# Performance work log

Measured on AMD Instinct MI355X. Metric: run time of the kernel, lower is better.

## Reference

```python
import jax, jax.numpy as jnp
import numpy as np

H = 8  # number of heads


def setup_inputs() -> dict:
    key0 = jax.random.key(0)
    ks = jax.random.split(key0, 10)
    B, Lq, Lk = 2, 256, 512
    q_model = k_model = v_model = d_model = 512
    d_k = d_model // H
    s = 0.02
    return {
        "query": jax.random.normal(ks[0], (B, Lq, q_model), jnp.float32),
        "key": jax.random.normal(ks[1], (B, Lk, k_model), jnp.float32),
        "value": jax.random.normal(ks[2], (B, Lk, v_model), jnp.float32),
        "mask": jax.random.randint(ks[3], (B, Lk), 0, 2, jnp.int32),
        # weights stored as (in, out) so projection is x @ W
        "Wq": jax.random.normal(ks[4], (q_model, d_model), jnp.float32) * s,
        "Wk": jax.random.normal(ks[5], (k_model, d_model), jnp.float32) * s,
        "Wv": jax.random.normal(ks[6], (v_model, d_model), jnp.float32) * s,
        "Wo": jax.random.normal(ks[7], (d_model, d_model), jnp.float32) * s,
        "wa": jax.random.normal(ks[8], (d_k,), jnp.float32) * s,
    }


def reference(query, key, value, mask, Wq, Wk, Wv, Wo, wa):
    B, Lq, _ = query.shape
    Lk = key.shape[1]
    d_model = Wq.shape[1]
    d_k = d_model // H

    def split_heads(x, W, L):
        return (x @ W).reshape(B, L, H, d_k).transpose(0, 2, 1, 3)  # (B,H,L,dk)

    q = split_heads(query, Wq, Lq)
    k = split_heads(key, Wk, Lk)
    v = split_heads(value, Wv, Lk)

    # additive (Bahdanau) scores: tanh(q_i + k_j) . wa  -> (B,H,Lq,Lk)
    feats = jnp.tanh(q[:, :, :, None, :] + k[:, :, None, :, :])
    scores = jnp.einsum("bhqkd,d->bhqk", feats, wa)

    scores = jnp.where(mask[:, None, None, :] == 0, jnp.float32(-1e9), scores)
    weights = jax.nn.softmax(scores, axis=-1)

    x = jnp.einsum("bhqk,bhkd->bhqd", weights, v)
    x = x.transpose(0, 2, 1, 3).reshape(B, Lq, H * d_k)
    return x @ Wo
```

## Files before the change

kernel.cpp:

```cpp
#include <hip/hip_runtime.h>

#define NB 2
#define LQ 256
#define LK 512
#define DM 512
#define NH 8
#define ROWS 4
#define C2F 2.885390081777927f
#define L2E 1.4426950408889634f

typedef __attribute__((ext_vector_type(8))) short short8;
typedef __attribute__((ext_vector_type(4))) float f32x4;

__device__ __forceinline__ ushort f2bf(float x) {
    unsigned int u = __float_as_uint(x);
    unsigned int r = (u + 0x7fffu + ((u >> 16) & 1u)) >> 16;
    return (ushort)r;
}
__device__ __forceinline__ float bf2f(ushort u) {
    return __uint_as_float(((unsigned int)u) << 16);
}

__global__ __launch_bounds__(256) void cvt_in_kernel(
    const float* __restrict__ query, const float* __restrict__ key,
    const float* __restrict__ value, ushort* __restrict__ Ah, ushort* __restrict__ Al)
{
    int i4 = blockIdx.x * 256 + threadIdx.x;
    int i = i4 * 4;
    const float* src;
    if (i < 262144)       src = query + i;
    else if (i < 786432)  src = key + (i - 262144);
    else                  src = value + (i - 786432);
    float4 x = *reinterpret_cast<const float4*>(src);
    ushort h0 = f2bf(x.x), h1 = f2bf(x.y), h2 = f2bf(x.z), h3 = f2bf(x.w);
    ushort4 hv = make_ushort4(h0, h1, h2, h3);
    ushort4 lv = make_ushort4(f2bf(x.x - bf2f(h0)), f2bf(x.y - bf2f(h1)),
                              f2bf(x.z - bf2f(h2)), f2bf(x.w - bf2f(h3)));
    *reinterpret_cast<ushort4*>(&Ah[i]) = hv;
    *reinterpret_cast<ushort4*>(&Al[i]) = lv;
}

__global__ __launch_bounds__(256) void cvt_w_kernel(
    const float* __restrict__ Wq, const float* __restrict__ Wk,
    const float* __restrict__ Wv, const float* __restrict__ Wo,
    ushort* __restrict__ Wth, ushort* __restrict__ Wtl)
{
    __shared__ float T[32][33];
    const int widx = blockIdx.z;
    const float* W = (widx == 0) ? Wq : (widx == 1) ? Wk : (widx == 2) ? Wv : Wo;
    const int nt = blockIdx.x, kt = blockIdx.y;
    const int tid = threadIdx.x;
    const int rr = tid >> 3, c4 = tid & 7;
    float4 v = *reinterpret_cast<const float4*>(&W[(size_t)(kt * 32 + rr) * 512 + nt * 32 + c4 * 4]);
    T[c4 * 4 + 0][rr] = v.x;
    T[c4 * 4 + 1][rr] = v.y;
    T[c4 * 4 + 2][rr] = v.z;
    T[c4 * 4 + 3][rr] = v.w;
    __syncthreads();
    const int nr = tid >> 3, k4 = tid & 7;
    float x0 = T[nr][k4 * 4 + 0], x1 = T[nr][k4 * 4 + 1];
    float x2 = T[nr][k4 * 4 + 2], x3 = T[nr][k4 * 4 + 3];
    ushort h0 = f2bf(x0), h1 = f2bf(x1), h2 = f2bf(x2), h3 = f2bf(x3);
    size_t o = (size_t)widx * 262144 + (size_t)(nt * 32 + nr) * 512 + kt * 32 + k4 * 4;
    *reinterpret_cast<ushort4*>(&Wth[o]) = make_ushort4(h0, h1, h2, h3);
    *reinterpret_cast<ushort4*>(&Wtl[o]) = make_ushort4(
        f2bf(x0 - bf2f(h0)), f2bf(x1 - bf2f(h1)), f2bf(x2 - bf2f(h2)), f2bf(x3 - bf2f(h3)));
}

__device__ __forceinline__ void gemm64_bf16(
    const ushort* __restrict__ Ah, const ushort* __restrict__ Al, int arow0,
    const ushort* __restrict__ Bth, const ushort* __restrict__ Btl,
    float* __restrict__ C, int crow0, int col0)
{
    __shared__ __align__(16) ushort AsH[64 * 40];
    __shared__ __align__(16) ushort AsL[64 * 40];
    __shared__ __align__(16) ushort BsH[64 * 40];
    __shared__ __align__(16) ushort BsL[64 * 40];
    const int tid = threadIdx.x;
    const int lane = tid & 63;
    const int w = tid >> 6, wr = w >> 1, wc = w & 1;
    const int srow = tid >> 2, sk8 = (tid & 3) * 8;

    f32x4 acc[2][2];
    #pragma unroll
    for (int i = 0; i < 2; ++i)
        #pragma unroll
        for (int j = 0; j < 2; ++j) acc[i][j] = (f32x4)0.0f;

    const int fr_row = (lane & 15), fk8 = (lane >> 4) * 8;

    for (int k0 = 0; k0 < 512; k0 += 32) {
        short8 gah = *reinterpret_cast<const short8*>(&Ah[(size_t)(arow0 + srow) * 512 + k0 + sk8]);
        short8 gal = *reinterpret_cast<const short8*>(&Al[(size_t)(arow0 + srow) * 512 + k0 + sk8]);
        short8 gbh = *reinterpret_cast<const short8*>(&Bth[(size_t)(col0 + srow) * 512 + k0 + sk8]);
        short8 gbl = *reinterpret_cast<const short8*>(&Btl[(size_t)(col0 + srow) * 512 + k0 + sk8]);
        __syncthreads();
        *reinterpret_cast<short8*>(&AsH[srow * 40 + sk8]) = gah;
        *reinterpret_cast<short8*>(&AsL[srow * 40 + sk8]) = gal;
        *reinterpret_cast<short8*>(&BsH[srow * 40 + sk8]) = gbh;
        *reinterpret_cast<short8*>(&BsL[srow * 40 + sk8]) = gbl;
        __syncthreads();
        short8 ah[2], al[2], bh[2], bl[2];
        #pragma unroll
        for (int fr = 0; fr < 2; ++fr) {
            int r = wr * 32 + fr * 16 + fr_row;
            ah[fr] = *reinterpret_cast<const short8*>(&AsH[r * 40 + fk8]);
            al[fr] = *reinterpret_cast<const short8*>(&AsL[r * 40 + fk8]);
        }
        #pragma unroll
        for (int fc = 0; fc < 2; ++fc) {
            int n = wc * 32 + fc * 16 + fr_row;
            bh[fc] = *reinterpret_cast<const short8*>(&BsH[n * 40 + fk8]);
            bl[fc] = *reinterpret_cast<const short8*>(&BsL[n * 40 + fk8]);
        }
        #pragma unroll
        for (int fr = 0; fr < 2; ++fr)
            #pragma unroll
            for (int fc = 0; fc < 2; ++fc) {
                acc[fr][fc] = __builtin_amdgcn_mfma_f32_16x16x32_bf16(ah[fr], bh[fc], acc[fr][fc], 0, 0, 0);
                acc[fr][fc] = __builtin_amdgcn_mfma_f32_16x16x32_bf16(ah[fr], bl[fc], acc[fr][fc], 0, 0, 0);
                acc[fr][fc] = __builtin_amdgcn_mfma_f32_16x16x32_bf16(al[fr], bh[fc], acc[fr][fc], 0, 0, 0);
            }
    }
    #pragma unroll
    for (int fr = 0; fr < 2; ++fr)
        #pragma unroll
        for (int fc = 0; fc < 2; ++fc)
            #pragma unroll
            for (int i = 0; i < 4; ++i) {
                int r = crow0 + wr * 32 + fr * 16 + (lane >> 4) * 4 + i;
                int c = col0 + wc * 32 + fc * 16 + (lane & 15);
                C[(size_t)r * 512 + c] = acc[fr][fc][i];
            }
}

__global__ __launch_bounds__(256) void qkv_gemm_kernel(
    const ushort* __restrict__ Ah, const ushort* __restrict__ Al,
    const ushort* __restrict__ Wth, const ushort* __restrict__ Wtl,
    float* __restrict__ Qb, float* __restrict__ Kb, float* __restrict__ Vb)
{
    const int rb = blockIdx.y, cb = blockIdx.x;
    int row0 = rb * 64;
    const ushort* bh; const ushort* bl; float* C; int crow0;
    if (row0 < 512)       { bh = Wth;           bl = Wtl;           C = Qb; crow0 = row0; }
    else if (row0 < 1536) { bh = Wth + 262144;  bl = Wtl + 262144;  C = Kb; crow0 = row0 - 512; }
    else                  { bh = Wth + 524288;  bl = Wtl + 524288;  C = Vb; crow0 = row0 - 1536; }
    gemm64_bf16(Ah, Al, row0, bh, bl, C, crow0, cb * 64);
}

__global__ __launch_bounds__(256) void out_gemm_kernel(
    const ushort* __restrict__ xh, const ushort* __restrict__ xl,
    const ushort* __restrict__ Woh, const ushort* __restrict__ Wol,
    float* __restrict__ out)
{
    gemm64_bf16(xh, xl, blockIdx.y * 64, Woh, Wol, out, blockIdx.y * 64, blockIdx.x * 64);
}

__global__ __launch_bounds__(256) void attn_kernel(
    const float* __restrict__ Qb, const float* __restrict__ Kb,
    const float* __restrict__ Vb, const int* __restrict__ mask,
    const float* __restrict__ wa,
    ushort* __restrict__ xh, ushort* __restrict__ xl)
{
    __shared__ float qs[ROWS][64];
    __shared__ float was[64];
    __shared__ float wsm[ROWS][512];
    __shared__ float red[ROWS][8];
    __shared__ float xp[4][ROWS][64];

    const int tid = threadIdx.x;
    const int lane = tid & 63;
    const int w = tid >> 6;
    const int bid = blockIdx.x;
    const int qt = bid & 63;
    const int h = (bid >> 6) & 7;
    const int b = bid >> 9;
    const int q0 = qt * ROWS;

    if (tid < ROWS * 64) {
        int r = tid >> 6, d = tid & 63;
        qs[r][d] = Qb[(size_t)(b * LQ + q0 + r) * DM + h * 64 + d] * C2F;
    }
    if (tid < 64) was[tid] = wa[tid];
    __syncthreads();

    const float* Kh = Kb + ((size_t)b * LK) * DM + h * 64;
    const int jb = w * 128;
    const float* K0p = Kh + (size_t)(jb + lane) * DM;
    const float* K1p = K0p + (size_t)64 * DM;

    float s[ROWS][2];
    #pragma unroll
    for (int r = 0; r < ROWS; ++r) { s[r][0] = 0.0f; s[r][1] = 0.0f; }

    for (int db = 0; db < 8; ++db) {
        const int d0 = db * 8;
        float4 kA0 = *reinterpret_cast<const float4*>(&K0p[d0]);
        float4 kA1 = *reinterpret_cast<const float4*>(&K0p[d0 + 4]);
        float4 kB0 = *reinterpret_cast<const float4*>(&K1p[d0]);
        float4 kB1 = *reinterpret_cast<const float4*>(&K1p[d0 + 4]);
        float kc0[8], kc1[8], wav[8];
        kc0[0] = kA0.x * C2F; kc0[1] = kA0.y * C2F; kc0[2] = kA0.z * C2F; kc0[3] = kA0.w * C2F;
        kc0[4] = kA1.x * C2F; kc0[5] = kA1.y * C2F; kc0[6] = kA1.z * C2F; kc0[7] = kA1.w * C2F;
        kc1[0] = kB0.x * C2F; kc1[1] = kB0.y * C2F; kc1[2] = kB0.z * C2F; kc1[3] = kB0.w * C2F;
        kc1[4] = kB1.x * C2F; kc1[5] = kB1.y * C2F; kc1[6] = kB1.z * C2F; kc1[7] = kB1.w * C2F;
        float4 wv0 = *reinterpret_cast<const float4*>(&was[d0]);
        float4 wv1 = *reinterpret_cast<const float4*>(&was[d0 + 4]);
        wav[0] = wv0.x; wav[1] = wv0.y; wav[2] = wv0.z; wav[3] = wv0.w;
        wav[4] = wv1.x; wav[5] = wv1.y; wav[6] = wv1.z; wav[7] = wv1.w;
        #pragma unroll
        for (int r = 0; r < ROWS; ++r) {
            float4 q0f = *reinterpret_cast<const float4*>(&qs[r][d0]);
            float4 q1f = *reinterpret_cast<const float4*>(&qs[r][d0 + 4]);
            float qv[8];
            qv[0] = q0f.x; qv[1] = q0f.y; qv[2] = q0f.z; qv[3] = q0f.w;
            qv[4] = q1f.x; qv[5] = q1f.y; qv[6] = q1f.z; qv[7] = q1f.w;
            #pragma unroll
            for (int dd = 0; dd < 8; ++dd) {
                float e0 = __builtin_amdgcn_exp2f(qv[dd] + kc0[dd]);
                float r0 = __builtin_amdgcn_rcpf(1.0f + e0);
                float t0 = fmaf(-2.0f, r0, 1.0f);
                s[r][0] = fmaf(t0, wav[dd], s[r][0]);
                float e1 = __builtin_amdgcn_exp2f(qv[dd] + kc1[dd]);
                float r1 = __builtin_amdgcn_rcpf(1.0f + e1);
                float t1 = fmaf(-2.0f, r1, 1.0f);
                s[r][1] = fmaf(t1, wav[dd], s[r][1]);
            }
        }
    }

    const int* mb = mask + b * LK;
    int m0 = mb[jb + lane], m1 = mb[jb + 64 + lane];
    #pragma unroll
    for (int r = 0; r < ROWS; ++r) {
        if (m0 == 0) s[r][0] = -1e9f;
        if (m1 == 0) s[r][1] = -1e9f;
    }

    #pragma unroll
    for (int r = 0; r < ROWS; ++r) {
        float mx = fmaxf(s[r][0], s[r][1]);
        #pragma unroll
        for (int off = 32; off > 0; off >>= 1) mx = fmaxf(mx, __shfl_xor(mx, off));
        if (lane == 0) red[r][w] = mx;
    }
    __syncthreads();
    float p[ROWS][2];
    #pragma unroll
    for (int r = 0; r < ROWS; ++r) {
        float gmx = fmaxf(fmaxf(red[r][0], red[r][1]), fmaxf(red[r][2], red[r][3]));
        p[r][0] = __builtin_amdgcn_exp2f((s[r][0] - gmx) * L2E);
        p[r][1] = __builtin_amdgcn_exp2f((s[r][1] - gmx) * L2E);
        float sm = p[r][0] + p[r][1];
        #pragma unroll
        for (int off = 32; off > 0; off >>= 1) sm += __shfl_xor(sm, off);
        if (lane == 0) red[r][4 + w] = sm;
    }
    __syncthreads();
    #pragma unroll
    for (int r = 0; r < ROWS; ++r) {
        float tot = (red[r][4] + red[r][5]) + (red[r][6] + red[r][7]);
        float inv = __builtin_amdgcn_rcpf(tot);
        wsm[r][jb + lane] = p[r][0] * inv;
        wsm[r][jb + 64 + lane] = p[r][1] * inv;
    }
    __syncthreads();

    const float* Vh = Vb + ((size_t)b * LK) * DM + h * 64;
    float o0 = 0.0f, o1 = 0.0f, o2 = 0.0f, o3 = 0.0f;
    const int jq = w * 128;
    #pragma unroll 4
    for (int jj = 0; jj < 128; jj += 4) {
        const int j = jq + jj;
        float4 w0 = *reinterpret_cast<const float4*>(&wsm[0][j]);
        float4 w1 = *reinterpret_cast<const float4*>(&wsm[1][j]);
        float4 w2 = *reinterpret_cast<const float4*>(&wsm[2][j]);
        float4 w3 = *reinterpret_cast<const float4*>(&wsm[3][j]);
        float v0 = Vh[(size_t)(j + 0) * DM + lane];
        float v1 = Vh[(size_t)(j + 1) * DM + lane];
        float v2 = Vh[(size_t)(j + 2) * DM + lane];
        float v3 = Vh[(size_t)(j + 3) * DM + lane];
        o0 = fmaf(w0.x, v0, o0); o0 = fmaf(w0.y, v1, o0); o0 = fmaf(w0.z, v2, o0); o0 = fmaf(w0.w, v3, o0);
        o1 = fmaf(w1.x, v0, o1); o1 = fmaf(w1.y, v1, o1); o1 = fmaf(w1.z, v2, o1); o1 = fmaf(w1.w, v3, o1);
        o2 = fmaf(w2.x, v0, o2); o2 = fmaf(w2.y, v1, o2); o2 = fmaf(w2.z, v2, o2); o2 = fmaf(w2.w, v3, o2);
        o3 = fmaf(w3.x, v0, o3); o3 = fmaf(w3.y, v1, o3); o3 = fmaf(w3.z, v2, o3); o3 = fmaf(w3.w, v3, o3);
    }
    xp[w][0][lane] = o0;
    xp[w][1][lane] = o1;
    xp[w][2][lane] = o2;
    xp[w][3][lane] = o3;
    __syncthreads();
    {
        const int r = w;
        float acc = ((xp[0][r][lane] + xp[1][r][lane]) + (xp[2][r][lane] + xp[3][r][lane]));
        size_t oidx = (size_t)(b * LQ + q0 + r) * DM + h * 64 + lane;
        ushort hb = f2bf(acc);
        xh[oidx] = hb;
        xl[oidx] = f2bf(acc - bf2f(hb));
    }
}

extern "C" void kernel_launch(void* const* d_in, const int* in_sizes, int n_in,
                              void* d_out, int out_size, void* d_ws, size_t ws_size,
                              hipStream_t stream)
{
    const float* query = (const float*)d_in[0];
    const float* key   = (const float*)d_in[1];
    const float* value = (const float*)d_in[2];
    const int*   mask  = (const int*)d_in[3];
    const float* Wq    = (const float*)d_in[4];
    const float* Wk    = (const float*)d_in[5];
    const float* Wv    = (const float*)d_in[6];
    const float* Wo    = (const float*)d_in[7];
    const float* wa    = (const float*)d_in[8];
    float* out = (float*)d_out;

    char* W = (char*)d_ws;
    float*  Qb  = (float*)(W);
    float*  Kb  = (float*)(W + 1048576);
    float*  Vb  = (float*)(W + 3145728);
    ushort* Ah  = (ushort*)(W + 5242880);
    ushort* Al  = (ushort*)(W + 7864320);
    ushort* Wth = (ushort*)(W + 10485760);
    ushort* Wtl = (ushort*)(W + 12582912);
    ushort* xh  = (ushort*)(W + 14680064);
    ushort* xl  = (ushort*)(W + 15204352);

    cvt_in_kernel<<<dim3(1280), 256, 0, stream>>>(query, key, value, Ah, Al);
    cvt_w_kernel<<<dim3(16, 16, 4), 256, 0, stream>>>(Wq, Wk, Wv, Wo, Wth, Wtl);
    qkv_gemm_kernel<<<dim3(8, 40), 256, 0, stream>>>(Ah, Al, Wth, Wtl, Qb, Kb, Vb);
    attn_kernel<<<dim3(1024), 256, 0, stream>>>(Qb, Kb, Vb, mask, wa, xh, xl);
    out_gemm_kernel<<<dim3(8, 8), 256, 0, stream>>>(xh, xl, Wth + 786432, Wtl + 786432, out);
}
```

Before: 140.6 us.

## Compact masked keys, fuse prep kernels, and use per-wave GEMM tiles

Merges the input and weight conversion kernels with a new pass that compacts the unmasked key indices per batch. Attention then computes tanh scores only for valid keys and gathers V rows by index, skipping the masked half of the additive-score work. The tanh is reformulated so the constant term folds into a precomputed sum of wa, and the C2F scale moves into the QKV GEMM epilogue. The GEMMs switch from LDS-tiled 64x64 blocks to independent per-wave 16x16 tiles read straight from global memory, and attention uses 2 query rows per block instead of 4. This adds an extra gather indirection and gives up LDS data reuse in the GEMMs.

```diff
diff --git a/kernel.cpp b/kernel.cpp
--- a/kernel.cpp
+++ b/kernel.cpp
@@ -5,7 +5,6 @@
 #define LK 512
 #define DM 512
 #define NH 8
-#define ROWS 4
 #define C2F 2.885390081777927f
 #define L2E 1.4426950408889634f
 
@@ -21,117 +20,96 @@
     return __uint_as_float(((unsigned int)u) << 16);
 }
 
-__global__ __launch_bounds__(256) void cvt_in_kernel(
+__global__ __launch_bounds__(256) void prep_kernel(
     const float* __restrict__ query, const float* __restrict__ key,
-    const float* __restrict__ value, ushort* __restrict__ Ah, ushort* __restrict__ Al)
-{
-    int i4 = blockIdx.x * 256 + threadIdx.x;
-    int i = i4 * 4;
-    const float* src;
-    if (i < 262144)       src = query + i;
-    else if (i < 786432)  src = key + (i - 262144);
-    else                  src = value + (i - 786432);
-    float4 x = *reinterpret_cast<const float4*>(src);
-    ushort h0 = f2bf(x.x), h1 = f2bf(x.y), h2 = f2bf(x.z), h3 = f2bf(x.w);
-    ushort4 hv = make_ushort4(h0, h1, h2, h3);
-    ushort4 lv = make_ushort4(f2bf(x.x - bf2f(h0)), f2bf(x.y - bf2f(h1)),
-                              f2bf(x.z - bf2f(h2)), f2bf(x.w - bf2f(h3)));
-    *reinterpret_cast<ushort4*>(&Ah[i]) = hv;
-    *reinterpret_cast<ushort4*>(&Al[i]) = lv;
-}
-
-__global__ __launch_bounds__(256) void cvt_w_kernel(
+    const float* __restrict__ value, const int* __restrict__ mask,
     const float* __restrict__ Wq, const float* __restrict__ Wk,
     const float* __restrict__ Wv, const float* __restrict__ Wo,
-    ushort* __restrict__ Wth, ushort* __restrict__ Wtl)
+    ushort* __restrict__ Ah, ushort* __restrict__ Al,
+    ushort* __restrict__ Wth, ushort* __restrict__ Wtl,
+    int* __restrict__ vidx, int* __restrict__ nvarr)
 {
     __shared__ float T[32][33];
-    const int widx = blockIdx.z;
-    const float* W = (widx == 0) ? Wq : (widx == 1) ? Wk : (widx == 2) ? Wv : Wo;
-    const int nt = blockIdx.x, kt = blockIdx.y;
+    const int blk = blockIdx.x;
     const int tid = threadIdx.x;
-    const int rr = tid >> 3, c4 = tid & 7;
-    float4 v = *reinterpret_cast<const float4*>(&W[(size_t)(kt * 32 + rr) * 512 + nt * 32 + c4 * 4]);
-    T[c4 * 4 + 0][rr] = v.x;
-    T[c4 * 4 + 1][rr] = v.y;
-    T[c4 * 4 + 2][rr] = v.z;
-    T[c4 * 4 + 3][rr] = v.w;
-    __syncthreads();
-    const int nr = tid >> 3, k4 = tid & 7;
-    float x0 = T[nr][k4 * 4 + 0], x1 = T[nr][k4 * 4 + 1];
-    float x2 = T[nr][k4 * 4 + 2], x3 = T[nr][k4 * 4 + 3];
-    ushort h0 = f2bf(x0), h1 = f2bf(x1), h2 = f2bf(x2), h3 = f2bf(x3);
-    size_t o = (size_t)widx * 262144 + (size_t)(nt * 32 + nr) * 512 + kt * 32 + k4 * 4;
-    *reinterpret_cast<ushort4*>(&Wth[o]) = make_ushort4(h0, h1, h2, h3);
-    *reinterpret_cast<ushort4*>(&Wtl[o]) = make_ushort4(
-        f2bf(x0 - bf2f(h0)), f2bf(x1 - bf2f(h1)), f2bf(x2 - bf2f(h2)), f2bf(x3 - bf2f(h3)));
-}
-
-__device__ __forceinline__ void gemm64_bf16(
+
+    if (blk < 1280) {
+        int i = (blk * 256 + tid) * 4;
+        const float* src;
+        if (i < 262144)       src = query + i;
+        else if (i < 786432)  src = key + (i - 262144);
+        else                  src = value + (i - 786432);
+        float4 x = *reinterpret_cast<const float4*>(src);
+        ushort h0 = f2bf(x.x), h1 = f2bf(x.y), h2 = f2bf(x.z), h3 = f2bf(x.w);
+        *reinterpret_cast<ushort4*>(&Ah[i]) = make_ushort4(h0, h1, h2, h3);
+        *reinterpret_cast<ushort4*>(&Al[i]) = make_ushort4(
+            f2bf(x.x - bf2f(h0)), f2bf(x.y - bf2f(h1)),
+            f2bf(x.z - bf2f(h2)), f2bf(x.w - bf2f(h3)));
+    } else if (blk < 2304) {
+        const int bid2 = blk - 1280;
+        const int widx = bid2 >> 8;
+        const int kt = (bid2 >> 4) & 15, nt = bid2 & 15;
+        const float* W = (widx == 0) ? Wq : (widx == 1) ? Wk : (widx == 2) ? Wv : Wo;
+        const int rr = tid >> 3, c4 = tid & 7;
+        float4 v = *reinterpret_cast<const float4*>(&W[(size_t)(kt * 32 + rr) * 512 + nt * 32 + c4 * 4]);
+        T[c4 * 4 + 0][rr] = v.x;
+        T[c4 * 4 + 1][rr] = v.y;
+        T[c4 * 4 + 2][rr] = v.z;
+        T[c4 * 4 + 3][rr] = v.w;
+        __syncthreads();
+        const int nr = tid >> 3, k4 = tid & 7;
+        float x0 = T[nr][k4 * 4 + 0], x1 = T[nr][k4 * 4 + 1];
+        float x2 = T[nr][k4 * 4 + 2], x3 = T[nr][k4 * 4 + 3];
+        ushort h0 = f2bf(x0), h1 = f2bf(x1), h2 = f2bf(x2), h3 = f2bf(x3);
+        size_t o = (size_t)widx * 262144 + (size_t)(nt * 32 + nr) * 512 + kt * 32 + k4 * 4;
+        *reinterpret_cast<ushort4*>(&Wth[o]) = make_ushort4(h0, h1, h2, h3);
+        *reinterpret_cast<ushort4*>(&Wtl[o]) = make_ushort4(
+            f2bf(x0 - bf2f(h0)), f2bf(x1 - bf2f(h1)), f2bf(x2 - bf2f(h2)), f2bf(x3 - bf2f(h3)));
+    } else {
+        const int b = blk - 2304;
+        if (tid < 64) {
+            const int lane = tid;
+            const int* mb = mask + b * LK;
+            int base = 0;
+            #pragma unroll
+            for (int it = 0; it < 8; ++it) {
+                int j = it * 64 + lane;
+                bool m = mb[j] != 0;
+                unsigned long long bal = __ballot(m);
+                int pos = base + (int)__popcll(bal & ((1ull << lane) - 1ull));
+                if (m) vidx[b * 512 + pos] = j;
+                base += (int)__popcll(bal);
+            }
+            for (int j = base + lane; j < 512; j += 64) vidx[b * 512 + j] = 0;
+            if (lane == 0) nvarr[b] = base;
+        }
+    }
+}
+
+__device__ __forceinline__ void wave_gemm16(
     const ushort* __restrict__ Ah, const ushort* __restrict__ Al, int arow0,
-    const ushort* __restrict__ Bth, const ushort* __restrict__ Btl,
-    float* __restrict__ C, int crow0, int col0)
-{
-    __shared__ __align__(16) ushort AsH[64 * 40];
-    __shared__ __align__(16) ushort AsL[64 * 40];
-    __shared__ __align__(16) ushort BsH[64 * 40];
-    __shared__ __align__(16) ushort BsL[64 * 40];
-    const int tid = threadIdx.x;
-    const int lane = tid & 63;
-    const int w = tid >> 6, wr = w >> 1, wc = w & 1;
-    const int srow = tid >> 2, sk8 = (tid & 3) * 8;
-
-    f32x4 acc[2][2];
-    #pragma unroll
-    for (int i = 0; i < 2; ++i)
-        #pragma unroll
-        for (int j = 0; j < 2; ++j) acc[i][j] = (f32x4)0.0f;
-
-    const int fr_row = (lane & 15), fk8 = (lane >> 4) * 8;
-
+    const ushort* __restrict__ Bth, const ushort* __restrict__ Btl, int ncol0,
+    float* __restrict__ C, int crow0, float scale, int lane)
+{
+    const int fr = lane & 15, k8 = (lane >> 4) * 8;
+    const ushort* aph = Ah + (size_t)(arow0 + fr) * 512 + k8;
+    const ushort* apl = Al + (size_t)(arow0 + fr) * 512 + k8;
+    const ushort* bph = Bth + (size_t)(ncol0 + fr) * 512 + k8;
+    const ushort* bpl = Btl + (size_t)(ncol0 + fr) * 512 + k8;
+    f32x4 acc = (f32x4)0.0f;
+    #pragma unroll 4
     for (int k0 = 0; k0 < 512; k0 += 32) {
-        short8 gah = *reinterpret_cast<const short8*>(&Ah[(size_t)(arow0 + srow) * 512 + k0 + sk8]);
-        short8 gal = *reinterpret_cast<const short8*>(&Al[(size_t)(arow0 + srow) * 512 + k0 + sk8]);
-        short8 gbh = *reinterpret_cast<const short8*>(&Bth[(size_t)(col0 + srow) * 512 + k0 + sk8]);
-        short8 gbl = *reinterpret_cast<const short8*>(&Btl[(size_t)(col0 + srow) * 512 + k0 + sk8]);
-        __syncthreads();
-        *reinterpret_cast<short8*>(&AsH[srow * 40 + sk8]) = gah;
-        *reinterpret_cast<short8*>(&AsL[srow * 40 + sk8]) = gal;
-        *reinterpret_cast<short8*>(&BsH[srow * 40 + sk8]) = gbh;
-        *reinterpret_cast<short8*>(&BsL[srow * 40 + sk8]) = gbl;
-        __syncthreads();
-        short8 ah[2], al[2], bh[2], bl[2];
-        #pragma unroll
-        for (int fr = 0; fr < 2; ++fr) {
-            int r = wr * 32 + fr * 16 + fr_row;
-            ah[fr] = *reinterpret_cast<const short8*>(&AsH[r * 40 + fk8]);
-            al[fr] = *reinterpret_cast<const short8*>(&AsL[r * 40 + fk8]);
-        }
-        #pragma unroll
-        for (int fc = 0; fc < 2; ++fc) {
-            int n = wc * 32 + fc * 16 + fr_row;
-            bh[fc] = *reinterpret_cast<const short8*>(&BsH[n * 40 + fk8]);
-            bl[fc] = *reinterpret_cast<const short8*>(&BsL[n * 40 + fk8]);
-        }
-        #pragma unroll
-        for (int fr = 0; fr < 2; ++fr)
-            #pragma unroll
-            for (int fc = 0; fc < 2; ++fc) {
-                acc[fr][fc] = __builtin_amdgcn_mfma_f32_16x16x32_bf16(ah[fr], bh[fc], acc[fr][fc], 0, 0, 0);
-                acc[fr][fc] = __builtin_amdgcn_mfma_f32_16x16x32_bf16(ah[fr], bl[fc], acc[fr][fc], 0, 0, 0);
-                acc[fr][fc] = __builtin_amdgcn_mfma_f32_16x16x32_bf16(al[fr], bh[fc], acc[fr][fc], 0, 0, 0);
-            }
-    }
-    #pragma unroll
-    for (int fr = 0; fr < 2; ++fr)
-        #pragma unroll
-        for (int fc = 0; fc < 2; ++fc)
-            #pragma unroll
-            for (int i = 0; i < 4; ++i) {
-                int r = crow0 + wr * 32 + fr * 16 + (lane >> 4) * 4 + i;
-                int c = col0 + wc * 32 + fc * 16 + (lane & 15);
-                C[(size_t)r * 512 + c] = acc[fr][fc][i];
-            }
+        short8 a_h = *reinterpret_cast<const short8*>(aph + k0);
+        short8 a_l = *reinterpret_cast<const short8*>(apl + k0);
+        short8 b_h = *reinterpret_cast<const short8*>(bph + k0);
+        short8 b_l = *reinterpret_cast<const short8*>(bpl + k0);
+        acc = __builtin_amdgcn_mfma_f32_16x16x32_bf16(a_h, b_h, acc, 0, 0, 0);
+        acc = __builtin_amdgcn_mfma_f32_16x16x32_bf16(a_h, b_l, acc, 0, 0, 0);
+        acc = __builtin_amdgcn_mfma_f32_16x16x32_bf16(a_l, b_h, acc, 0, 0, 0);
+    }
+    #pragma unroll
+    for (int i = 0; i < 4; ++i)
+        C[(size_t)(crow0 + (lane >> 4) * 4 + i) * 512 + ncol0 + fr] = acc[i] * scale;
 }
 
 __global__ __launch_bounds__(256) void qkv_gemm_kernel(
@@ -139,13 +117,14 @@
     const ushort* __restrict__ Wth, const ushort* __restrict__ Wtl,
     float* __restrict__ Qb, float* __restrict__ Kb, float* __restrict__ Vb)
 {
-    const int rb = blockIdx.y, cb = blockIdx.x;
-    int row0 = rb * 64;
-    const ushort* bh; const ushort* bl; float* C; int crow0;
-    if (row0 < 512)       { bh = Wth;           bl = Wtl;           C = Qb; crow0 = row0; }
-    else if (row0 < 1536) { bh = Wth + 262144;  bl = Wtl + 262144;  C = Kb; crow0 = row0 - 512; }
-    else                  { bh = Wth + 524288;  bl = Wtl + 524288;  C = Vb; crow0 = row0 - 1536; }
-    gemm64_bf16(Ah, Al, row0, bh, bl, C, crow0, cb * 64);
+    const int gw = (blockIdx.x * 256 + threadIdx.x) >> 6;
+    const int lane = threadIdx.x & 63;
+    const int mt = gw >> 5, nt = gw & 31;
+    const ushort* bth; const ushort* btl; float* C; int crow0; float scale;
+    if (mt < 32)      { bth = Wth;          btl = Wtl;          C = Qb; crow0 = mt * 16;        scale = C2F; }
+    else if (mt < 96) { bth = Wth + 262144; btl = Wtl + 262144; C = Kb; crow0 = (mt - 32) * 16; scale = C2F; }
+    else              { bth = Wth + 524288; btl = Wtl + 524288; C = Vb; crow0 = (mt - 96) * 16; scale = 1.0f; }
+    wave_gemm16(Ah, Al, mt * 16, bth, btl, nt * 16, C, crow0, scale, lane);
 }
 
 __global__ __launch_bounds__(256) void out_gemm_kernel(
@@ -153,101 +132,102 @@
     const ushort* __restrict__ Woh, const ushort* __restrict__ Wol,
     float* __restrict__ out)
 {
-    gemm64_bf16(xh, xl, blockIdx.y * 64, Woh, Wol, out, blockIdx.y * 64, blockIdx.x * 64);
-}
+    const int gw = (blockIdx.x * 256 + threadIdx.x) >> 6;
+    const int lane = threadIdx.x & 63;
+    const int mt = gw >> 5, nt = gw & 31;
+    wave_gemm16(xh, xl, mt * 16, Woh, Wol, nt * 16, out, mt * 16, 1.0f, lane);
+}
+
+#define SCOP(QV, KV, WV, U) { \
+    float e_ = __builtin_amdgcn_exp2f((QV) + (KV)); \
+    float r_ = __builtin_amdgcn_rcpf(1.0f + e_); \
+    (U) = fmaf((WV), r_, (U)); }
 
 __global__ __launch_bounds__(256) void attn_kernel(
     const float* __restrict__ Qb, const float* __restrict__ Kb,
-    const float* __restrict__ Vb, const int* __restrict__ mask,
-    const float* __restrict__ wa,
+    const float* __restrict__ Vb, const float* __restrict__ wa,
+    const int* __restrict__ vidx, const int* __restrict__ nvarr,
     ushort* __restrict__ xh, ushort* __restrict__ xl)
 {
-    __shared__ float qs[ROWS][64];
+    __shared__ float qs[2][64];
     __shared__ float was[64];
-    __shared__ float wsm[ROWS][512];
-    __shared__ float red[ROWS][8];
-    __shared__ float xp[4][ROWS][64];
+    __shared__ float wsm[2][512];
+    __shared__ float red[2][8];
+    __shared__ float xp[4][2][64];
+    __shared__ int vlds[512];
+    __shared__ int nv_s;
 
     const int tid = threadIdx.x;
     const int lane = tid & 63;
     const int w = tid >> 6;
     const int bid = blockIdx.x;
-    const int qt = bid & 63;
-    const int h = (bid >> 6) & 7;
-    const int b = bid >> 9;
-    const int q0 = qt * ROWS;
-
-    if (tid < ROWS * 64) {
+    const int qt = bid & 127;
+    const int h = (bid >> 7) & 7;
+    const int b = bid >> 10;
+    const int q0 = qt * 2;
+
+    if (tid < 128) {
         int r = tid >> 6, d = tid & 63;
-        qs[r][d] = Qb[(size_t)(b * LQ + q0 + r) * DM + h * 64 + d] * C2F;
+        qs[r][d] = Qb[(size_t)(b * LQ + q0 + r) * DM + h * 64 + d];
     }
     if (tid < 64) was[tid] = wa[tid];
-    __syncthreads();
+    vlds[tid] = vidx[b * 512 + tid];
+    vlds[tid + 256] = vidx[b * 512 + tid + 256];
+    if (tid == 0) nv_s = nvarr[b];
+    __syncthreads();
+    const int nv = nv_s;
+
+    float swa = was[lane];
+    #pragma unroll
+    for (int off = 32; off > 0; off >>= 1) swa += __shfl_xor(swa, off);
 
     const float* Kh = Kb + ((size_t)b * LK) * DM + h * 64;
-    const int jb = w * 128;
-    const float* K0p = Kh + (size_t)(jb + lane) * DM;
-    const float* K1p = K0p + (size_t)64 * DM;
-
-    float s[ROWS][2];
-    #pragma unroll
-    for (int r = 0; r < ROWS; ++r) { s[r][0] = 0.0f; s[r][1] = 0.0f; }
-
-    for (int db = 0; db < 8; ++db) {
-        const int d0 = db * 8;
-        float4 kA0 = *reinterpret_cast<const float4*>(&K0p[d0]);
-        float4 kA1 = *reinterpret_cast<const float4*>(&K0p[d0 + 4]);
-        float4 kB0 = *reinterpret_cast<const float4*>(&K1p[d0]);
-        float4 kB1 = *reinterpret_cast<const float4*>(&K1p[d0 + 4]);
-        float kc0[8], kc1[8], wav[8];
-        kc0[0] = kA0.x * C2F; kc0[1] = kA0.y * C2F; kc0[2] = kA0.z * C2F; kc0[3] = kA0.w * C2F;
-        kc0[4] = kA1.x * C2F; kc0[5] = kA1.y * C2F; kc0[6] = kA1.z * C2F; kc0[7] = kA1.w * C2F;
-        kc1[0] = kB0.x * C2F; kc1[1] = kB0.y * C2F; kc1[2] = kB0.z * C2F; kc1[3] = kB0.w * C2F;
-        kc1[4] = kB1.x * C2F; kc1[5] = kB1.y * C2F; kc1[6] = kB1.z * C2F; kc1[7] = kB1.w * C2F;
-        float4 wv0 = *reinterpret_cast<const float4*>(&was[d0]);
-        float4 wv1 = *reinterpret_cast<const float4*>(&was[d0 + 4]);
-        wav[0] = wv0.x; wav[1] = wv0.y; wav[2] = wv0.z; wav[3] = wv0.w;
-        wav[4] = wv1.x; wav[5] = wv1.y; wav[6] = wv1.z; wav[7] = wv1.w;
+    float s[2][2];
+
+    #pragma unroll
+    for (int c = 0; c < 2; ++c) {
+        const int sbase = c * 256 + w * 64;
+        if (sbase >= nv) { s[0][c] = -1e9f; s[1][c] = -1e9f; continue; }
+        const int slot = sbase + lane;
+        const bool act = slot < nv;
+        const int row = vlds[slot];
+        const float* Kp = Kh + (size_t)row * DM;
+        float u0 = 0.0f, u1 = 0.0f;
         #pragma unroll
-        for (int r = 0; r < ROWS; ++r) {
-            float4 q0f = *reinterpret_cast<const float4*>(&qs[r][d0]);
-            float4 q1f = *reinterpret_cast<const float4*>(&qs[r][d0 + 4]);
-            float qv[8];
-            qv[0] = q0f.x; qv[1] = q0f.y; qv[2] = q0f.z; qv[3] = q0f.w;
-            qv[4] = q1f.x; qv[5] = q1f.y; qv[6] = q1f.z; qv[7] = q1f.w;
-            #pragma unroll
-            for (int dd = 0; dd < 8; ++dd) {
-                float e0 = __builtin_amdgcn_exp2f(qv[dd] + kc0[dd]);
-                float r0 = __builtin_amdgcn_rcpf(1.0f + e0);
-                float t0 = fmaf(-2.0f, r0, 1.0f);
-                s[r][0] = fmaf(t0, wav[dd], s[r][0]);
-                float e1 = __builtin_amdgcn_exp2f(qv[dd] + kc1[dd]);
-                float r1 = __builtin_amdgcn_rcpf(1.0f + e1);
-                float t1 = fmaf(-2.0f, r1, 1.0f);
-                s[r][1] = fmaf(t1, wav[dd], s[r][1]);
-            }
+        for (int db = 0; db < 8; ++db) {
+            const int d0 = db * 8;
+            float4 kA = *reinterpret_cast<const float4*>(&Kp[d0]);
+            float4 kB = *reinterpret_cast<const float4*>(&Kp[d0 + 4]);
+            float4 qA0 = *reinterpret_cast<const float4*>(&qs[0][d0]);
+            float4 qB0 = *reinterpret_cast<const float4*>(&qs[0][d0 + 4]);
+            float4 qA1 = *reinterpret_cast<const float4*>(&qs[1][d0]);
+            float4 qB1 = *reinterpret_cast<const float4*>(&qs[1][d0 + 4]);
+            float4 wA = *reinterpret_cast<const float4*>(&was[d0]);
+            float4 wB = *reinterpret_cast<const float4*>(&was[d0 + 4]);
+            SCOP(qA0.x, kA.x, wA.x, u0)  SCOP(qA1.x, kA.x, wA.x, u1)
+            SCOP(qA0.y, kA.y, wA.y, u0)  SCOP(qA1.y, kA.y, wA.y, u1)
+            SCOP(qA0.z, kA.z, wA.z, u0)  SCOP(qA1.z, kA.z, wA.z, u1)
+            SCOP(qA0.w, kA.w, wA.w, u0)  SCOP(qA1.w, kA.w, wA.w, u1)
+            SCOP(qB0.x, kB.x, wB.x, u0)  SCOP(qB1.x, kB.x, wB.x, u1)
+            SCOP(qB0.y, kB.y, wB.y, u0)  SCOP(qB1.y, kB.y, wB.y, u1)
+            SCOP(qB0.z, kB.z, wB.z, u0)  SCOP(qB1.z, kB.z, wB.z, u1)
+            SCOP(qB0.w, kB.w, wB.w, u0)  SCOP(qB1.w, kB.w, wB.w, u1)
         }
-    }
-
-    const int* mb = mask + b * LK;
-    int m0 = mb[jb + lane], m1 = mb[jb + 64 + lane];
-    #pragma unroll
-    for (int r = 0; r < ROWS; ++r) {
-        if (m0 == 0) s[r][0] = -1e9f;
-        if (m1 == 0) s[r][1] = -1e9f;
-    }
-
-    #pragma unroll
-    for (int r = 0; r < ROWS; ++r) {
+        s[0][c] = act ? fmaf(-2.0f, u0, swa) : -1e9f;
+        s[1][c] = act ? fmaf(-2.0f, u1, swa) : -1e9f;
+    }
+
+    #pragma unroll
+    for (int r = 0; r < 2; ++r) {
         float mx = fmaxf(s[r][0], s[r][1]);
         #pragma unroll
         for (int off = 32; off > 0; off >>= 1) mx = fmaxf(mx, __shfl_xor(mx, off));
         if (lane == 0) red[r][w] = mx;
     }
     __syncthreads();
-    float p[ROWS][2];
-    #pragma unroll
-    for (int r = 0; r < ROWS; ++r) {
+    float p[2][2];
+    #pragma unroll
+    for (int r = 0; r < 2; ++r) {
         float gmx = fmaxf(fmaxf(red[r][0], red[r][1]), fmaxf(red[r][2], red[r][3]));
         p[r][0] = __builtin_amdgcn_exp2f((s[r][0] - gmx) * L2E);
         p[r][1] = __builtin_amdgcn_exp2f((s[r][1] - gmx) * L2E);
@@ -258,41 +238,37 @@
     }
     __syncthreads();
     #pragma unroll
-    for (int r = 0; r < ROWS; ++r) {
+    for (int r = 0; r < 2; ++r) {
         float tot = (red[r][4] + red[r][5]) + (red[r][6] + red[r][7]);
         float inv = __builtin_amdgcn_rcpf(tot);
-        wsm[r][jb + lane] = p[r][0] * inv;
-        wsm[r][jb + 64 + lane] = p[r][1] * inv;
+        wsm[r][w * 64 + lane] = p[r][0] * inv;
+        wsm[r][256 + w * 64 + lane] = p[r][1] * inv;
     }
     __syncthreads();
 
     const float* Vh = Vb + ((size_t)b * LK) * DM + h * 64;
-    float o0 = 0.0f, o1 = 0.0f, o2 = 0.0f, o3 = 0.0f;
-    const int jq = w * 128;
-    #pragma unroll 4
-    for (int jj = 0; jj < 128; jj += 4) {
-        const int j = jq + jj;
-        float4 w0 = *reinterpret_cast<const float4*>(&wsm[0][j]);
-        float4 w1 = *reinterpret_cast<const float4*>(&wsm[1][j]);
-        float4 w2 = *reinterpret_cast<const float4*>(&wsm[2][j]);
-        float4 w3 = *reinterpret_cast<const float4*>(&wsm[3][j]);
-        float v0 = Vh[(size_t)(j + 0) * DM + lane];
-        float v1 = Vh[(size_t)(j + 1) * DM + lane];
-        float v2 = Vh[(size_t)(j + 2) * DM + lane];
-        float v3 = Vh[(size_t)(j + 3) * DM + lane];
-        o0 = fmaf(w0.x, v0, o0); o0 = fmaf(w0.y, v1, o0); o0 = fmaf(w0.z, v2, o0); o0 = fmaf(w0.w, v3, o0);
-        o1 = fmaf(w1.x, v0, o1); o1 = fmaf(w1.y, v1, o1); o1 = fmaf(w1.z, v2, o1); o1 = fmaf(w1.w, v3, o1);
-        o2 = fmaf(w2.x, v0, o2); o2 = fmaf(w2.y, v1, o2); o2 = fmaf(w2.z, v2, o2); o2 = fmaf(w2.w, v3, o2);
-        o3 = fmaf(w3.x, v0, o3); o3 = fmaf(w3.y, v1, o3); o3 = fmaf(w3.z, v2, o3); o3 = fmaf(w3.w, v3, o3);
+    float o0 = 0.0f, o1 = 0.0f;
+    const int ngr = (nv + 3) >> 2;
+    for (int gi = w; gi < ngr; gi += 4) {
+        const int sb = gi * 4;
+        float4 w0 = *reinterpret_cast<const float4*>(&wsm[0][sb]);
+        float4 w1 = *reinterpret_cast<const float4*>(&wsm[1][sb]);
+        int j0 = vlds[sb + 0], j1 = vlds[sb + 1], j2 = vlds[sb + 2], j3 = vlds[sb + 3];
+        float v0 = Vh[(size_t)j0 * DM + lane];
+        float v1 = Vh[(size_t)j1 * DM + lane];
+        float v2 = Vh[(size_t)j2 * DM + lane];
+        float v3 = Vh[(size_t)j3 * DM + lane];
+        o0 = fmaf(w0.x, v0, o0); o0 = fmaf(w0.y, v1, o0);
+        o0 = fmaf(w0.z, v2, o0); o0 = fmaf(w0.w, v3, o0);
+        o1 = fmaf(w1.x, v0, o1); o1 = fmaf(w1.y, v1, o1);
+        o1 = fmaf(w1.z, v2, o1); o1 = fmaf(w1.w, v3, o1);
     }
     xp[w][0][lane] = o0;
     xp[w][1][lane] = o1;
-    xp[w][2][lane] = o2;
-    xp[w][3][lane] = o3;
-    __syncthreads();
-    {
+    __syncthreads();
+    if (w < 2) {
         const int r = w;
-        float acc = ((xp[0][r][lane] + xp[1][r][lane]) + (xp[2][r][lane] + xp[3][r][lane]));
+        float acc = (xp[0][r][lane] + xp[1][r][lane]) + (xp[2][r][lane] + xp[3][r][lane]);
         size_t oidx = (size_t)(b * LQ + q0 + r) * DM + h * 64 + lane;
         ushort hb = f2bf(acc);
         xh[oidx] = hb;
@@ -316,19 +292,21 @@
     float* out = (float*)d_out;
 
     char* W = (char*)d_ws;
-    float*  Qb  = (float*)(W);
-    float*  Kb  = (float*)(W + 1048576);
-    float*  Vb  = (float*)(W + 3145728);
-    ushort* Ah  = (ushort*)(W + 5242880);
-    ushort* Al  = (ushort*)(W + 7864320);
-    ushort* Wth = (ushort*)(W + 10485760);
-    ushort* Wtl = (ushort*)(W + 12582912);
-    ushort* xh  = (ushort*)(W + 14680064);
-    ushort* xl  = (ushort*)(W + 15204352);
-
-    cvt_in_kernel<<<dim3(1280), 256, 0, stream>>>(query, key, value, Ah, Al);
-    cvt_w_kernel<<<dim3(16, 16, 4), 256, 0, stream>>>(Wq, Wk, Wv, Wo, Wth, Wtl);
-    qkv_gemm_kernel<<<dim3(8, 40), 256, 0, stream>>>(Ah, Al, Wth, Wtl, Qb, Kb, Vb);
-    attn_kernel<<<dim3(1024), 256, 0, stream>>>(Qb, Kb, Vb, mask, wa, xh, xl);
-    out_gemm_kernel<<<dim3(8, 8), 256, 0, stream>>>(xh, xl, Wth + 786432, Wtl + 786432, out);
-}
+    float*  Qb    = (float*)(W);
+    float*  Kb    = (float*)(W + 1048576);
+    float*  Vb    = (float*)(W + 3145728);
+    ushort* Ah    = (ushort*)(W + 5242880);
+    ushort* Al    = (ushort*)(W + 7864320);
+    ushort* Wth   = (ushort*)(W + 10485760);
+    ushort* Wtl   = (ushort*)(W + 12582912);
+    ushort* xh    = (ushort*)(W + 14680064);
+    ushort* xl    = (ushort*)(W + 15204352);
+    int*    vidx  = (int*)(W + 15728640);
+    int*    nvarr = (int*)(W + 15732736);
+
+    prep_kernel<<<dim3(2306), 256, 0, stream>>>(query, key, value, mask,
+                                                Wq, Wk, Wv, Wo, Ah, Al, Wth, Wtl, vidx, nvarr);
+    qkv_gemm_kernel<<<dim3(1280), 256, 0, stream>>>(Ah, Al, Wth, Wtl, Qb, Kb, Vb);
+    attn_kernel<<<dim3(2048), 256, 0, stream>>>(Qb, Kb, Vb, wa, vidx, nvarr, xh, xl);
+    out_gemm_kernel<<<dim3(256), 256, 0, stream>>>(xh, xl, Wth + 786432, Wtl + 786432, out);
+}
```

Result: slower. 161.8 us (+15.0%).
